# Kernel tuning notes

Measured on AMD Instinct MI355X. Metric: run time of the kernel, lower is better.

Reference implementation:

```python
import jax, jax.numpy as jnp
import numpy as np

DN = ('NCHW', 'OIHW', 'NCHW')

def conv3x3(x, w):
    # stride-1, SAME padding, no bias (matches build_conv_layer(..., 3, stride=1, padding='same', bias=False))
    return jax.lax.conv_general_dilated(x, w, window_strides=(1, 1), padding='SAME', dimension_numbers=DN)

def setup_inputs() -> dict:
    key = jax.random.key(0)
    k1, k2, k3, k4 = jax.random.split(key, 4)
    B, C, H, W = 4, 256, 64, 64
    inputs = jax.random.normal(k1, (B, C, H, W), dtype=jnp.float32)
    ref = jax.random.normal(k2, (B, C, H, W), dtype=jnp.float32)
    # xavier-uniform-ish conv weights, [O, I, kH, kW]
    fan = C * 9
    lim = np.sqrt(6.0 / (fan + fan)).astype(np.float32)
    w1 = jax.random.uniform(k3, (C, C, 3, 3), dtype=jnp.float32, minval=-lim, maxval=lim)
    w2 = jax.random.uniform(k4, (C, C, 3, 3), dtype=jnp.float32, minval=-lim, maxval=lim)
    gamma = jnp.float32(0.5)
    return {'inputs': inputs, 'ref': ref, 'w1': w1, 'w2': w2, 'gamma': gamma}

def reference(inputs, ref, w1, w2, gamma):
    # Faithful to source: x0 = relu(conv1(inputs)) is computed then immediately
    # overwritten by a view of x1 (a bug in the original), so inputs only
    # contributes its shape. We execute the dead conv for FLOP parity.
    _dead = jax.nn.relu(conv3x3(inputs, w1))
    x1 = jax.nn.relu(conv3x3(ref, w1))            # [B, C, H, W]
    B, C, H, W = x1.shape
    q = x1.transpose(0, 2, 3, 1).reshape(B, H * W, C)   # [B, HW, C]
    k = x1.reshape(B, C, H * W)                          # [B, C, HW]
    scores = jnp.einsum('bnc,bcm->bnm', q, k)            # [B, HW, HW]
    corr = jax.nn.softmax(scores, axis=1)                # softmax over dim=1 (atypical axis)
    v = jax.nn.relu(conv3x3(ref, w2)).reshape(B, C, H * W)  # [B, C, HW]
    A = jnp.einsum('bcn,bnm->bcm', v, corr).reshape(inputs.shape)
    return A * gamma + ref
```

## Files before the change

kernel.cpp:

```cpp
#include <hip/hip_runtime.h>
#include <math.h>

#define CDIM 256
#define NSEQ 4096
#define HWDIM 64
#define PPIX 4356

typedef unsigned short u16;
typedef __attribute__((ext_vector_type(8))) short bf16x8;
typedef __attribute__((ext_vector_type(4))) float f32x4;
typedef __attribute__((ext_vector_type(16))) float f32x16;

__device__ __forceinline__ u16 f2bf(float f) {
    unsigned u = __float_as_uint(f);
    unsigned r = (u + 0x7FFFu + ((u >> 16) & 1u)) >> 16;
    return (u16)r;
}

__device__ __forceinline__ void gload_lds16(const u16* g, u16* l) {
    __builtin_amdgcn_global_load_lds(
        (const __attribute__((address_space(1))) unsigned int*)g,
        (__attribute__((address_space(3))) unsigned int*)l, 16, 0, 0);
}

__global__ __launch_bounds__(256)
void pad_transpose_kernel(const float* __restrict__ x, u16* __restrict__ padded)
{
    __shared__ float lds[64 * 65];
    const int tid = threadIdx.x;
    const int y = blockIdx.x, c0 = blockIdx.y << 6, b = blockIdx.z;
    #pragma unroll
    for (int i = 0; i < 16; ++i) {
        int f = tid + (i << 8);
        int c = f >> 6, xx = f & 63;
        lds[c * 65 + xx] = x[(((size_t)(b * CDIM + c0 + c)) * HWDIM + y) * HWDIM + xx];
    }
    __syncthreads();
    #pragma unroll
    for (int i = 0; i < 2; ++i) {
        int f = tid + (i << 8);
        int xx = f >> 3, c8 = f & 7;
        union { u16 h[8]; float4 v; } pk;
        #pragma unroll
        for (int j = 0; j < 8; ++j) pk.h[j] = f2bf(lds[(c8 * 8 + j) * 65 + xx]);
        *(float4*)&padded[((size_t)b * PPIX + (y + 1) * 66 + (xx + 1)) * CDIM + c0 + (c8 << 3)] = pk.v;
    }
}

__global__ __launch_bounds__(256)
void w_prepack2_kernel(const float* __restrict__ w1, const float* __restrict__ w2,
                       u16* __restrict__ wk1, u16* __restrict__ wk2)
{
    int g = (blockIdx.x << 8) + threadIdx.x;
    int t = g & 65535;
    const float* wp = (g < 65536 ? w1 : w2) + (size_t)t * 9;
    u16* wk = (g < 65536 ? wk1 : wk2);
    #pragma unroll
    for (int j = 0; j < 9; ++j) wk[j * 65536 + t] = f2bf(wp[j]);
}

#define CW1_OFF 8192
#define CW2_OFF 24576

__device__ __forceinline__ void conv_stage2(const u16* __restrict__ padded,
                                            const u16* __restrict__ wk1,
                                            const u16* __restrict__ wk2,
                                            u16* Xb, u16* W1b, u16* W2b,
                                            int b, int y0, int cb, int t,
                                            int wv, int lane)
{
    const int kyx = t >> 2, cib = (t & 3) << 6;
    const int ky = kyx / 3, kx = kyx - ky * 3;
    #pragma unroll
    for (int i = 0; i < 2; ++i) {
        int f = ((i << 2) + wv) << 6;
        int fl = f + lane;
        int r = fl >> 3;
        int gsw = (fl & 7) ^ (r & 7);
        gload_lds16(&padded[((size_t)b * PPIX + (y0 + ky) * 66 + r + kx) * CDIM + cib + (gsw << 3)],
                    Xb + (f << 3));
    }
    #pragma unroll
    for (int i = 0; i < 4; ++i) {
        int f = ((i << 2) + wv) << 6;
        int fl = f + lane;
        int r = fl >> 3;
        int gsw = (fl & 7) ^ (r & 7);
        gload_lds16(&wk1[((size_t)kyx << 16) + (size_t)(cb + r) * 256 + cib + (gsw << 3)],
                    W1b + (f << 3));
    }
    #pragma unroll
    for (int i = 0; i < 4; ++i) {
        int f = ((i << 2) + wv) << 6;
        int fl = f + lane;
        int r = fl >> 3;
        int gsw = (fl & 7) ^ (r & 7);
        gload_lds16(&wk2[((size_t)kyx << 16) + (size_t)(cb + r) * 256 + cib + (gsw << 3)],
                    W2b + (f << 3));
    }
}

__global__ __launch_bounds__(256)
void conv_dual_kernel(const u16* __restrict__ padded,
                      const u16* __restrict__ wk1, const u16* __restrict__ wk2,
                      u16* __restrict__ XT, u16* __restrict__ Vn)
{
    __shared__ alignas(16) u16 smem[40960];

    const int tid = threadIdx.x;
    const int lane = tid & 63, wv = tid >> 6;
    const int lr = lane & 15, lg = lane >> 4;
    const int cb = blockIdx.x << 7;
    const int y0 = blockIdx.y;
    const int b = blockIdx.z;

    f32x4 acc1[2][4] = {};
    f32x4 acc2[4][2] = {};

    conv_stage2(padded, wk1, wk2, smem, smem + CW1_OFF, smem + CW2_OFF,
                b, y0, cb, 0, wv, lane);
    __syncthreads();

    int cur = 0;
    for (int t = 0; t < 36; ++t) {
        if (t + 1 < 36)
            conv_stage2(padded, wk1, wk2, smem + (cur ^ 1) * 4096,
                        smem + CW1_OFF + (cur ^ 1) * 8192,
                        smem + CW2_OFF + (cur ^ 1) * 8192,
                        b, y0, cb, t + 1, wv, lane);

        const u16* Xs  = smem + cur * 4096;
        const u16* Ws1 = smem + CW1_OFF + cur * 8192;
        const u16* Ws2 = smem + CW2_OFF + cur * 8192;

        #pragma unroll
        for (int kk = 0; kk < 2; ++kk) {
            const int ca = ((kk << 5) + (lg << 3)) ^ ((lr & 7) << 3);
            bf16x8 xs[4];
            #pragma unroll
            for (int nf = 0; nf < 4; ++nf)
                xs[nf] = *(const bf16x8*)&Xs[((nf * 16 + lr) << 6) + ca];
            bf16x8 w1f[2], w2f[2];
            #pragma unroll
            for (int mf = 0; mf < 2; ++mf) {
                w1f[mf] = *(const bf16x8*)&Ws1[((wv * 32 + mf * 16 + lr) << 6) + ca];
                w2f[mf] = *(const bf16x8*)&Ws2[((wv * 32 + mf * 16 + lr) << 6) + ca];
            }
            #pragma unroll
            for (int mf = 0; mf < 2; ++mf)
                #pragma unroll
                for (int nf = 0; nf < 4; ++nf)
                    acc1[mf][nf] = __builtin_amdgcn_mfma_f32_16x16x32_bf16(w1f[mf], xs[nf], acc1[mf][nf], 0, 0, 0);
            #pragma unroll
            for (int mf = 0; mf < 4; ++mf)
                #pragma unroll
                for (int nf = 0; nf < 2; ++nf)
                    acc2[mf][nf] = __builtin_amdgcn_mfma_f32_16x16x32_bf16(xs[mf], w2f[nf], acc2[mf][nf], 0, 0, 0);
        }
        __syncthreads();
        cur ^= 1;
    }

    const int m0 = y0 << 6;
    #pragma unroll
    for (int mf = 0; mf < 2; ++mf)
        #pragma unroll
        for (int nf = 0; nf < 4; ++nf) {
            int cob = cb + wv * 32 + mf * 16 + lg * 4;
            int n = m0 + nf * 16 + lr;
            union { u16 h[4]; uint2 v; } pk;
            #pragma unroll
            for (int j = 0; j < 4; ++j) pk.h[j] = f2bf(fmaxf(acc1[mf][nf][j], 0.f));
            *(uint2*)&XT[((size_t)(b * NSEQ + n)) * CDIM + cob] = pk.v;
        }
    #pragma unroll
    for (int mf = 0; mf < 4; ++mf)
        #pragma unroll
        for (int nf = 0; nf < 2; ++nf) {
            int nb = m0 + mf * 16 + lg * 4;
            int co = cb + wv * 32 + nf * 16 + lr;
            union { u16 h[4]; uint2 v; } pk;
            #pragma unroll
            for (int j = 0; j < 4; ++j) pk.h[j] = f2bf(fmaxf(acc2[mf][nf][j], 0.f));
            *(uint2*)&Vn[((size_t)(b * CDIM + co)) * NSEQ + nb] = pk.v;
        }
}

__global__ __launch_bounds__(256)
void rownorm_kernel(const u16* __restrict__ XT, float* __restrict__ rn2,
                    float* __restrict__ bmax)
{
    __shared__ float wmax[4];
    const int tid = threadIdx.x;
    const int lane = tid & 63, wv = tid >> 6;
    const int row = (blockIdx.x << 2) + wv;
    const u16* xp = &XT[(size_t)row * CDIM + (lane << 2)];
    uint2 v = *(const uint2*)xp;
    float s = 0.f;
    #pragma unroll
    for (int j = 0; j < 4; ++j) {
        unsigned hu = (j & 1) ? ((&v.x)[j >> 1] >> 16) : ((&v.x)[j >> 1] & 0xFFFFu);
        float x = __uint_as_float(hu << 16);
        s += x * x;
    }
    #pragma unroll
    for (int off = 1; off < 64; off <<= 1) s += __shfl_xor(s, off);
    if (lane == 0) {
        rn2[row] = s;
        wmax[wv] = s;
    }
    __syncthreads();
    if (tid == 0)
        bmax[blockIdx.x] = fmaxf(fmaxf(wmax[0], wmax[1]), fmaxf(wmax[2], wmax[3]));
}

__global__ __launch_bounds__(256)
void maxred_kernel(const float* __restrict__ bmax, float* __restrict__ maxrn2)
{
    __shared__ float wred[4];
    const int tid = threadIdx.x;
    const int lane = tid & 63, wv = tid >> 6;
    const int b = blockIdx.x;
    float m = 0.f;
    #pragma unroll
    for (int i = 0; i < 4; ++i)
        m = fmaxf(m, bmax[(b << 10) + (i << 8) + tid]);
    #pragma unroll
    for (int off = 1; off < 64; off <<= 1) m = fmaxf(m, __shfl_xor(m, off));
    if (lane == 0) wred[wv] = m;
    __syncthreads();
    if (tid == 0)
        maxrn2[b] = fmaxf(fmaxf(wred[0], wred[1]), fmaxf(wred[2], wred[3]));
}

#define M_TILE 128
#define NC 64
#define NCHUNKS 32

#define KS_OFF 0
#define VS_OFF 32768
#define P_OFF  65536

__device__ __forceinline__ void stage_chunk(const u16* __restrict__ XT, const u16* __restrict__ Vn,
                                            u16* Kb, u16* Vb, int b, int n0, int wv, int lane)
{
    #pragma unroll
    for (int i = 0; i < 4; ++i) {
        int f = ((i << 3) + wv) << 6;
        int fl = f + lane;
        int r = fl >> 5;
        int gsw = (fl & 31) ^ (r & 15);
        gload_lds16(&XT[(size_t)(b * NSEQ + n0 + r) * CDIM + (gsw << 3)], Kb + (f << 3));
    }
    #pragma unroll
    for (int i = 0; i < 4; ++i) {
        int f = ((i << 3) + wv) << 6;
        int fl = f + lane;
        int r = fl >> 3;
        int gsw = (fl & 7) ^ (r & 7);
        gload_lds16(&Vn[(size_t)(b * CDIM + r) * NSEQ + n0 + (gsw << 3)], Vb + (f << 3));
    }
}

__global__ __launch_bounds__(512, 2)
void attn_part_kernel(const u16* __restrict__ XT, const u16* __restrict__ Vn,
                      const float* __restrict__ rn2, const float* __restrict__ maxrn2,
                      float* __restrict__ o0, u16* __restrict__ o1,
                      float* __restrict__ lsum)
{
    __shared__ alignas(16) u16 smem[73728];
    u16* Ps = smem + P_OFF;

    const int tid = threadIdx.x;
    const int lane = tid & 63;
    const int wv = tid >> 6;
    const int l31 = lane & 31;
    const int hi = lane >> 5;
    const int bh = blockIdx.x;
    const int b = bh >> 1, h = bh & 1;
    const int m0 = blockIdx.y * M_TILE;
    const int nbase = h * (NSEQ / 2);

    const int qt = wv & 3;
    const int kh = wv >> 2;
    const int qa = qt * 32 + l31;
    const int qsel = wv & 1;
    const int csel = wv >> 1;

    const float mq = sqrtf(rn2[(size_t)b * NSEQ + m0 + qa]) * sqrtf(maxrn2[b]);

    bf16x8 qreg[16];
    {
        const u16* qrow = &XT[(size_t)(b * NSEQ + m0 + qa) * CDIM + (hi << 3)];
        #pragma unroll
        for (int ks = 0; ks < 16; ++ks)
            qreg[ks] = *(const bf16x8*)(qrow + (ks << 4));
    }

    f32x16 o[2][2] = {};
    float lrun = 0.f;

    stage_chunk(XT, Vn, smem + KS_OFF, smem + VS_OFF, b, nbase, wv, lane);
    __syncthreads();

    int cur = 0;
    for (int ci = 0; ci < NCHUNKS; ++ci) {
        if (ci + 1 < NCHUNKS)
            stage_chunk(XT, Vn, smem + KS_OFF + (cur ^ 1) * 16384,
                        smem + VS_OFF + (cur ^ 1) * 16384,
                        b, nbase + (ci + 1) * NC, wv, lane);

        const u16* Kc = smem + KS_OFF + cur * 16384;
        const u16* Vc = smem + VS_OFF + cur * 16384;

        f32x16 s = {};
        {
            const int krow = kh * 32 + l31;
            const u16* kbase = &Kc[krow << 8];
            const int ksw = krow & 15;
            #pragma unroll
            for (int ks = 0; ks < 16; ++ks) {
                bf16x8 ka = *(const bf16x8*)&kbase[(((ks << 1) + hi) ^ ksw) << 3];
                s = __builtin_amdgcn_mfma_f32_32x32x16_bf16(ka, qreg[ks], s, 0, 0, 0);
            }
        }

        float p[16];
        float ps = 0.f;
        #pragma unroll
        for (int r = 0; r < 16; ++r) { p[r] = __expf(s[r] - mq); ps += p[r]; }
        ps += __shfl_xor(ps, 32);
        lrun += ps;

        {
            const int swz = qa & 7;
            #pragma unroll
            for (int r4 = 0; r4 < 4; ++r4) {
                union { u16 h4[4]; uint2 v; } pk;
                pk.h4[0] = f2bf(p[r4 * 4 + 0]); pk.h4[1] = f2bf(p[r4 * 4 + 1]);
                pk.h4[2] = f2bf(p[r4 * 4 + 2]); pk.h4[3] = f2bf(p[r4 * 4 + 3]);
                int g = (kh << 2) + r4;
                *(uint2*)&Ps[(qa << 6) + (((g ^ swz) << 3) | (hi << 2))] = pk.v;
            }
        }
        __syncthreads();

        {
            const int q0 = ((qsel << 1) + 0) * 32 + l31;
            const int q1 = ((qsel << 1) + 1) * 32 + l31;
            const int c0 = ((csel << 1) + 0) * 32 + l31;
            const int c1 = ((csel << 1) + 1) * 32 + l31;
            #pragma unroll
            for (int ks = 0; ks < 4; ++ks) {
                const int gp = (ks << 1) + hi;
                bf16x8 pb0 = *(const bf16x8*)&Ps[(q0 << 6) + ((gp ^ (q0 & 7)) << 3)];
                bf16x8 pb1 = *(const bf16x8*)&Ps[(q1 << 6) + ((gp ^ (q1 & 7)) << 3)];
                bf16x8 va0 = *(const bf16x8*)&Vc[(c0 << 6) + ((gp ^ (c0 & 7)) << 3)];
                bf16x8 va1 = *(const bf16x8*)&Vc[(c1 << 6) + ((gp ^ (c1 & 7)) << 3)];
                o[0][0] = __builtin_amdgcn_mfma_f32_32x32x16_bf16(va0, pb0, o[0][0], 0, 0, 0);
                o[0][1] = __builtin_amdgcn_mfma_f32_32x32x16_bf16(va1, pb0, o[0][1], 0, 0, 0);
                o[1][0] = __builtin_amdgcn_mfma_f32_32x32x16_bf16(va0, pb1, o[1][0], 0, 0, 0);
                o[1][1] = __builtin_amdgcn_mfma_f32_32x32x16_bf16(va1, pb1, o[1][1], 0, 0, 0);
            }
        }

        __syncthreads();
        cur ^= 1;
    }

    if (lane < 32)
        lsum[(size_t)(((h * 2 + kh) * 4 + b)) * NSEQ + m0 + qa] = lrun;

    #pragma unroll
    for (int qi = 0; qi < 2; ++qi) {
        const int q = m0 + ((qsel << 1) + qi) * 32 + l31;
        #pragma unroll
        for (int cj = 0; cj < 2; ++cj) {
            #pragma unroll
            for (int reg = 0; reg < 16; ++reg) {
                int c = ((csel << 1) + cj) * 32 + (reg & 3) + ((reg >> 2) << 3) + (hi << 2);
                size_t oi = ((size_t)(b * CDIM + c)) * NSEQ + q;
                if (h == 0) o0[oi] = o[qi][cj][reg];
                else        o1[oi] = f2bf(o[qi][cj][reg]);
            }
        }
    }
}

__global__ __launch_bounds__(256)
void merge_kernel(float* __restrict__ out, const u16* __restrict__ o1,
                  const float* __restrict__ lsum, const float* __restrict__ ref,
                  const float* __restrict__ gptr)
{
    const int f = (blockIdx.x << 8) + threadIdx.x;
    const int n4 = f & 1023;
    const int c = (f >> 10) & 255;
    const int b = f >> 18;
    const float g = gptr[0];

    float4 p0 = ((const float4*)out)[f];
    uint2 q1 = *(const uint2*)&o1[((size_t)(b * CDIM + c)) * NSEQ + (n4 << 2)];
    float4 rf = ((const float4*)ref)[f];

    float res[4];
    #pragma unroll
    for (int j = 0; j < 4; ++j) {
        int row = (n4 << 2) + j;
        float l = lsum[(size_t)(0 * 4 + b) * NSEQ + row]
                + lsum[(size_t)(1 * 4 + b) * NSEQ + row]
                + lsum[(size_t)(2 * 4 + b) * NSEQ + row]
                + lsum[(size_t)(3 * 4 + b) * NSEQ + row];
        float rl = 1.0f / l;
        float v0 = ((const float*)&p0)[j];
        unsigned hu = ((j & 1) ? ((&q1.x)[j >> 1] >> 16) : ((&q1.x)[j >> 1] & 0xFFFFu));
        float v1 = __uint_as_float(hu << 16);
        float a = (v0 + v1) * rl;
        res[j] = g * a + ((const float*)&rf)[j];
    }
    ((float4*)out)[f] = *(float4*)res;
}

extern "C" void kernel_launch(void* const* d_in, const int* in_sizes, int n_in,
                              void* d_out, int out_size, void* d_ws, size_t ws_size,
                              hipStream_t stream)
{
    const float* ref = (const float*)d_in[1];
    const float* w1  = (const float*)d_in[2];
    const float* w2  = (const float*)d_in[3];
    const float* gma = (const float*)d_in[4];
    float* out = (float*)d_out;

    u16* XT     = (u16*)d_ws;
    u16* Vn     = XT + (size_t)4 * NSEQ * CDIM;
    u16* padded = Vn + (size_t)4 * NSEQ * CDIM;
    u16* wk1    = padded + (size_t)4 * PPIX * CDIM;
    u16* wk2    = wk1 + (size_t)9 * 65536;
    u16*   o1     = padded;
    float* lsum   = (float*)wk1;
    float* rn2    = (float*)wk2;
    float* bmax   = rn2 + 16384;
    float* maxrn2 = bmax + 4096;

    hipMemsetAsync(padded, 0, (size_t)4 * PPIX * CDIM * sizeof(u16), stream);
    pad_transpose_kernel<<<dim3(64, 4, 4), 256, 0, stream>>>(ref, padded);
    w_prepack2_kernel<<<dim3(512), 256, 0, stream>>>(w1, w2, wk1, wk2);

    conv_dual_kernel<<<dim3(2, 64, 4), 256, 0, stream>>>(padded, wk1, wk2, XT, Vn);

    rownorm_kernel<<<dim3(4096), 256, 0, stream>>>(XT, rn2, bmax);
    maxred_kernel<<<dim3(4), 256, 0, stream>>>(bmax, maxrn2);

    attn_part_kernel<<<dim3(8, NSEQ / M_TILE), 512, 0, stream>>>(XT, Vn, rn2, maxrn2, out, o1, lsum);
    merge_kernel<<<dim3((4 * CDIM * NSEQ / 4) / 256), 256, 0, stream>>>(out, o1, lsum, ref, gma);
}
```

Before: 159.0 us.

## Warp-specialize attention into QK/softmax and PV wave groups with double-buffered P

Splits the 1024-thread block into two groups. Eight waves compute QK^T and the softmax numerators into a double-buffered P tile in LDS. The other eight waves stage V and run the PV MMAs one chunk behind, so the two phases run concurrently instead of back to back. This costs more LDS (160KB per block) and twice the threads per block, and it uses a 1024-thread launch bound that may force register spilling or cap occupancy at one block per CU.

```diff
diff --git a/kernel.cpp b/kernel.cpp
--- a/kernel.cpp
+++ b/kernel.cpp
@@ -237,12 +237,11 @@
 #define NC 64
 #define NCHUNKS 32
 
-#define KS_OFF 0
 #define VS_OFF 32768
 #define P_OFF  65536
 
-__device__ __forceinline__ void stage_chunk(const u16* __restrict__ XT, const u16* __restrict__ Vn,
-                                            u16* Kb, u16* Vb, int b, int n0, int wv, int lane)
+__device__ __forceinline__ void stage_K(const u16* __restrict__ XT, u16* Kb,
+                                        int b, int n0, int wv, int lane)
 {
     #pragma unroll
     for (int i = 0; i < 4; ++i) {
@@ -252,6 +251,11 @@
         int gsw = (fl & 31) ^ (r & 15);
         gload_lds16(&XT[(size_t)(b * NSEQ + n0 + r) * CDIM + (gsw << 3)], Kb + (f << 3));
     }
+}
+
+__device__ __forceinline__ void stage_V(const u16* __restrict__ Vn, u16* Vb,
+                                        int b, int n0, int wv, int lane)
+{
     #pragma unroll
     for (int i = 0; i < 4; ++i) {
         int f = ((i << 3) + wv) << 6;
@@ -262,18 +266,17 @@
     }
 }
 
-__global__ __launch_bounds__(512, 2)
+__global__ __launch_bounds__(1024, 4)
 void attn_part_kernel(const u16* __restrict__ XT, const u16* __restrict__ Vn,
                       const float* __restrict__ rn2, const float* __restrict__ maxrn2,
                       float* __restrict__ o0, u16* __restrict__ o1,
                       float* __restrict__ lsum)
 {
-    __shared__ alignas(16) u16 smem[73728];
-    u16* Ps = smem + P_OFF;
+    __shared__ alignas(16) u16 smem[81920];
 
     const int tid = threadIdx.x;
     const int lane = tid & 63;
-    const int wv = tid >> 6;
+    const int wid = tid >> 6;
     const int l31 = lane & 31;
     const int hi = lane >> 5;
     const int bh = blockIdx.x;
@@ -281,107 +284,117 @@
     const int m0 = blockIdx.y * M_TILE;
     const int nbase = h * (NSEQ / 2);
 
-    const int qt = wv & 3;
-    const int kh = wv >> 2;
-    const int qa = qt * 32 + l31;
-    const int qsel = wv & 1;
-    const int csel = wv >> 1;
-
-    const float mq = sqrtf(rn2[(size_t)b * NSEQ + m0 + qa]) * sqrtf(maxrn2[b]);
-
-    bf16x8 qreg[16];
-    {
-        const u16* qrow = &XT[(size_t)(b * NSEQ + m0 + qa) * CDIM + (hi << 3)];
+    if (wid < 8) {
+        const int qt = wid & 3;
+        const int kh = wid >> 2;
+        const int qa = qt * 32 + l31;
+
+        const float mq = sqrtf(rn2[(size_t)b * NSEQ + m0 + qa]) * sqrtf(maxrn2[b]);
+
+        bf16x8 qreg[16];
+        {
+            const u16* qrow = &XT[(size_t)(b * NSEQ + m0 + qa) * CDIM + (hi << 3)];
+            #pragma unroll
+            for (int ks = 0; ks < 16; ++ks)
+                qreg[ks] = *(const bf16x8*)(qrow + (ks << 4));
+        }
+        float lrun = 0.f;
+
+        stage_K(XT, smem, b, nbase, wid, lane);
+        __syncthreads();
+
+        for (int w = 0; w <= NCHUNKS; ++w) {
+            if (w < NCHUNKS) {
+                if (w + 1 < NCHUNKS)
+                    stage_K(XT, smem + ((w + 1) & 1) * 16384,
+                            b, nbase + (w + 1) * NC, wid, lane);
+
+                const u16* Kc = smem + (w & 1) * 16384;
+                u16* Pw = smem + P_OFF + (w & 1) * 8192;
+
+                f32x16 s = {};
+                {
+                    const int krow = kh * 32 + l31;
+                    const u16* kbase = &Kc[krow << 8];
+                    const int ksw = krow & 15;
+                    #pragma unroll
+                    for (int ks = 0; ks < 16; ++ks) {
+                        bf16x8 ka = *(const bf16x8*)&kbase[(((ks << 1) + hi) ^ ksw) << 3];
+                        s = __builtin_amdgcn_mfma_f32_32x32x16_bf16(ka, qreg[ks], s, 0, 0, 0);
+                    }
+                }
+
+                float p[16];
+                float ps = 0.f;
+                #pragma unroll
+                for (int r = 0; r < 16; ++r) { p[r] = __expf(s[r] - mq); ps += p[r]; }
+                ps += __shfl_xor(ps, 32);
+                lrun += ps;
+
+                const int swz = qa & 7;
+                #pragma unroll
+                for (int r4 = 0; r4 < 4; ++r4) {
+                    union { u16 h4[4]; uint2 v; } pk;
+                    pk.h4[0] = f2bf(p[r4 * 4 + 0]); pk.h4[1] = f2bf(p[r4 * 4 + 1]);
+                    pk.h4[2] = f2bf(p[r4 * 4 + 2]); pk.h4[3] = f2bf(p[r4 * 4 + 3]);
+                    int g = (kh << 2) + r4;
+                    *(uint2*)&Pw[(qa << 6) + (((g ^ swz) << 3) | (hi << 2))] = pk.v;
+                }
+            }
+            __syncthreads();
+        }
+
+        if (lane < 32)
+            lsum[(size_t)(((h * 2 + kh) * 4 + b)) * NSEQ + m0 + qa] = lrun;
+    } else {
+        const int pvw = wid - 8;
+        const int qsel = pvw & 1;
+        const int csel = pvw >> 1;
+
+        f32x16 o[2][2] = {};
+
+        __syncthreads();
+
+        for (int w = 0; w <= NCHUNKS; ++w) {
+            if (w < NCHUNKS)
+                stage_V(Vn, smem + VS_OFF + (w & 1) * 16384,
+                        b, nbase + w * NC, pvw, lane);
+            if (w >= 1) {
+                const u16* Vc = smem + VS_OFF + ((w - 1) & 1) * 16384;
+                const u16* Pc = smem + P_OFF + ((w - 1) & 1) * 8192;
+
+                const int q0 = ((qsel << 1) + 0) * 32 + l31;
+                const int q1 = ((qsel << 1) + 1) * 32 + l31;
+                const int c0 = ((csel << 1) + 0) * 32 + l31;
+                const int c1 = ((csel << 1) + 1) * 32 + l31;
+                #pragma unroll
+                for (int ks = 0; ks < 4; ++ks) {
+                    const int gp = (ks << 1) + hi;
+                    bf16x8 pb0 = *(const bf16x8*)&Pc[(q0 << 6) + ((gp ^ (q0 & 7)) << 3)];
+                    bf16x8 pb1 = *(const bf16x8*)&Pc[(q1 << 6) + ((gp ^ (q1 & 7)) << 3)];
+                    bf16x8 va0 = *(const bf16x8*)&Vc[(c0 << 6) + ((gp ^ (c0 & 7)) << 3)];
+                    bf16x8 va1 = *(const bf16x8*)&Vc[(c1 << 6) + ((gp ^ (c1 & 7)) << 3)];
+                    o[0][0] = __builtin_amdgcn_mfma_f32_32x32x16_bf16(va0, pb0, o[0][0], 0, 0, 0);
+                    o[0][1] = __builtin_amdgcn_mfma_f32_32x32x16_bf16(va1, pb0, o[0][1], 0, 0, 0);
+                    o[1][0] = __builtin_amdgcn_mfma_f32_32x32x16_bf16(va0, pb1, o[1][0], 0, 0, 0);
+                    o[1][1] = __builtin_amdgcn_mfma_f32_32x32x16_bf16(va1, pb1, o[1][1], 0, 0, 0);
+                }
+            }
+            __syncthreads();
+        }
+
         #pragma unroll
-        for (int ks = 0; ks < 16; ++ks)
-            qreg[ks] = *(const bf16x8*)(qrow + (ks << 4));
-    }
-
-    f32x16 o[2][2] = {};
-    float lrun = 0.f;
-
-    stage_chunk(XT, Vn, smem + KS_OFF, smem + VS_OFF, b, nbase, wv, lane);
-    __syncthreads();
-
-    int cur = 0;
-    for (int ci = 0; ci < NCHUNKS; ++ci) {
-        if (ci + 1 < NCHUNKS)
-            stage_chunk(XT, Vn, smem + KS_OFF + (cur ^ 1) * 16384,
-                        smem + VS_OFF + (cur ^ 1) * 16384,
-                        b, nbase + (ci + 1) * NC, wv, lane);
-
-        const u16* Kc = smem + KS_OFF + cur * 16384;
-        const u16* Vc = smem + VS_OFF + cur * 16384;
-
-        f32x16 s = {};
-        {
-            const int krow = kh * 32 + l31;
-            const u16* kbase = &Kc[krow << 8];
-            const int ksw = krow & 15;
-            #pragma unroll
-            for (int ks = 0; ks < 16; ++ks) {
-                bf16x8 ka = *(const bf16x8*)&kbase[(((ks << 1) + hi) ^ ksw) << 3];
-                s = __builtin_amdgcn_mfma_f32_32x32x16_bf16(ka, qreg[ks], s, 0, 0, 0);
-            }
-        }
-
-        float p[16];
-        float ps = 0.f;
-        #pragma unroll
-        for (int r = 0; r < 16; ++r) { p[r] = __expf(s[r] - mq); ps += p[r]; }
-        ps += __shfl_xor(ps, 32);
-        lrun += ps;
-
-        {
-            const int swz = qa & 7;
-            #pragma unroll
-            for (int r4 = 0; r4 < 4; ++r4) {
-                union { u16 h4[4]; uint2 v; } pk;
-                pk.h4[0] = f2bf(p[r4 * 4 + 0]); pk.h4[1] = f2bf(p[r4 * 4 + 1]);
-                pk.h4[2] = f2bf(p[r4 * 4 + 2]); pk.h4[3] = f2bf(p[r4 * 4 + 3]);
-                int g = (kh << 2) + r4;
-                *(uint2*)&Ps[(qa << 6) + (((g ^ swz) << 3) | (hi << 2))] = pk.v;
-            }
-        }
-        __syncthreads();
-
-        {
-            const int q0 = ((qsel << 1) + 0) * 32 + l31;
-            const int q1 = ((qsel << 1) + 1) * 32 + l31;
-            const int c0 = ((csel << 1) + 0) * 32 + l31;
-            const int c1 = ((csel << 1) + 1) * 32 + l31;
-            #pragma unroll
-            for (int ks = 0; ks < 4; ++ks) {
-                const int gp = (ks << 1) + hi;
-                bf16x8 pb0 = *(const bf16x8*)&Ps[(q0 << 6) + ((gp ^ (q0 & 7)) << 3)];
-                bf16x8 pb1 = *(const bf16x8*)&Ps[(q1 << 6) + ((gp ^ (q1 & 7)) << 3)];
-                bf16x8 va0 = *(const bf16x8*)&Vc[(c0 << 6) + ((gp ^ (c0 & 7)) << 3)];
-                bf16x8 va1 = *(const bf16x8*)&Vc[(c1 << 6) + ((gp ^ (c1 & 7)) << 3)];
-                o[0][0] = __builtin_amdgcn_mfma_f32_32x32x16_bf16(va0, pb0, o[0][0], 0, 0, 0);
-                o[0][1] = __builtin_amdgcn_mfma_f32_32x32x16_bf16(va1, pb0, o[0][1], 0, 0, 0);
-                o[1][0] = __builtin_amdgcn_mfma_f32_32x32x16_bf16(va0, pb1, o[1][0], 0, 0, 0);
-                o[1][1] = __builtin_amdgcn_mfma_f32_32x32x16_bf16(va1, pb1, o[1][1], 0, 0, 0);
-            }
-        }
-
-        __syncthreads();
-        cur ^= 1;
-    }
-
-    if (lane < 32)
-        lsum[(size_t)(((h * 2 + kh) * 4 + b)) * NSEQ + m0 + qa] = lrun;
-
-    #pragma unroll
-    for (int qi = 0; qi < 2; ++qi) {
-        const int q = m0 + ((qsel << 1) + qi) * 32 + l31;
-        #pragma unroll
-        for (int cj = 0; cj < 2; ++cj) {
-            #pragma unroll
-            for (int reg = 0; reg < 16; ++reg) {
-                int c = ((csel << 1) + cj) * 32 + (reg & 3) + ((reg >> 2) << 3) + (hi << 2);
-                size_t oi = ((size_t)(b * CDIM + c)) * NSEQ + q;
-                if (h == 0) o0[oi] = o[qi][cj][reg];
-                else        o1[oi] = f2bf(o[qi][cj][reg]);
+        for (int qi = 0; qi < 2; ++qi) {
+            const int q = m0 + ((qsel << 1) + qi) * 32 + l31;
+            #pragma unroll
+            for (int cj = 0; cj < 2; ++cj) {
+                #pragma unroll
+                for (int reg = 0; reg < 16; ++reg) {
+                    int c = ((csel << 1) + cj) * 32 + (reg & 3) + ((reg >> 2) << 3) + (hi << 2);
+                    size_t oi = ((size_t)(b * CDIM + c)) * NSEQ + q;
+                    if (h == 0) o0[oi] = o[qi][cj][reg];
+                    else        o1[oi] = f2bf(o[qi][cj][reg]);
+                }
             }
         }
     }
@@ -450,6 +463,6 @@
     rownorm_kernel<<<dim3(4096), 256, 0, stream>>>(XT, rn2, bmax);
     maxred_kernel<<<dim3(4), 256, 0, stream>>>(bmax, maxrn2);
 
-    attn_part_kernel<<<dim3(8, NSEQ / M_TILE), 512, 0, stream>>>(XT, Vn, rn2, maxrn2, out, o1, lsum);
+    attn_part_kernel<<<dim3(8, NSEQ / M_TILE), 1024, 0, stream>>>(XT, Vn, rn2, maxrn2, out, o1, lsum);
     merge_kernel<<<dim3((4 * CDIM * NSEQ / 4) / 256), 256, 0, stream>>>(out, o1, lsum, ref, gma);
 }
```

New measurement: 155.8 us. -2.1%, faster.
